# Performance work log

Measured on AMD Instinct MI355X. Metric: run time of the kernel, lower is better.

The kernel has to match this reference:

```python
import jax, jax.numpy as jnp
import numpy as np

HEADS = 8
DIM_HEAD = 64
GAMMA = 0.01
LAMBDA_REG = 0.001
EPS = 1e-6


def layer_norm(x, g, b, eps=1e-5):
    mu = x.mean(-1, keepdims=True)
    var = jnp.var(x, axis=-1, keepdims=True)
    return (x - mu) * jax.lax.rsqrt(var + eps) * g + b


def setup_inputs() -> dict:
    key = jax.random.key(0)
    ks = jax.random.split(key, 20)
    B, N, DIM = 8, 1024, 512
    d = DIM_HEAD
    inner = HEADS * d
    inp = {}
    inp["q"] = jax.random.normal(ks[0], (B, N, DIM), jnp.float32)
    inp["k"] = jax.random.normal(ks[1], (B, N, DIM), jnp.float32)
    inp["v"] = jax.random.normal(ks[2], (B, N, DIM), jnp.float32)
    # input_linear: LayerNorm(dim) + Linear(dim -> inner, no bias)
    inp["ln_g"] = jnp.ones((DIM,), jnp.float32)
    inp["ln_b"] = jnp.zeros((DIM,), jnp.float32)
    inp["W_in"] = jax.random.normal(ks[3], (DIM, inner), jnp.float32) * 0.02
    # weight_predictor: Linear(2d->d), LN(d), ReLU, Linear(d->d//2), ReLU, Linear(d//2->3), Softmax
    inp["wp_W1"] = jax.random.normal(ks[4], (2 * d, d), jnp.float32) * 0.05
    inp["wp_b1"] = jnp.zeros((d,), jnp.float32)
    inp["wp_ln_g"] = jnp.ones((d,), jnp.float32)
    inp["wp_ln_b"] = jnp.zeros((d,), jnp.float32)
    inp["wp_W2"] = jax.random.normal(ks[5], (d, d // 2), jnp.float32) * 0.05
    inp["wp_b2"] = jnp.zeros((d // 2,), jnp.float32)
    inp["wp_W3"] = jax.random.normal(ks[6], (d // 2, 3), jnp.float32) * 0.05
    inp["wp_b3"] = jnp.zeros((3,), jnp.float32)
    inp["weight_temp"] = jnp.ones((1,), jnp.float32) * 2.0
    # output_linear: Linear(inner -> dim) with bias
    inp["W_out"] = jax.random.normal(ks[7], (inner, DIM), jnp.float32) * 0.02
    inp["b_out"] = jnp.zeros((DIM,), jnp.float32)
    return inp


def reference(q, k, v, ln_g, ln_b, W_in, wp_W1, wp_b1, wp_ln_g, wp_ln_b,
              wp_W2, wp_b2, wp_W3, wp_b3, weight_temp, W_out, b_out):
    H, d = HEADS, DIM_HEAD
    B, N, _ = q.shape

    def proj(t):
        x = layer_norm(t, ln_g, ln_b) @ W_in          # [B, N, H*d]
        return x.reshape(B, N, H, d).transpose(2, 0, 1, 3)  # h q n d

    f_q, f_k, f_v = proj(q), proj(k), proj(v)
    m = f_k.shape[2]

    # --- cosine component (cosine_distance with clamp to [-0.95, 0.95]) ---
    dots_raw = jnp.einsum('hbnd,hbmd->hbnm', f_q, f_k)
    n1 = jnp.linalg.norm(f_q, axis=-1, keepdims=True) + EPS      # h b n 1
    n2 = jnp.linalg.norm(f_k, axis=-1) + EPS                      # h b m
    cosine_sim = jnp.clip(dots_raw / (n1 * n2[:, :, None, :]), -0.95, 0.95)

    # --- regularized covariance component ---
    f_k_c = f_k - f_k.mean(axis=2, keepdims=True)
    f_q_c = f_q - f_q.mean(axis=-1, keepdims=True)
    cov = jnp.einsum('hbnd,hbmd->hbnm', f_q_c, f_k_c) / (d ** 0.5 + 1e-6)
    cov = jnp.clip((LAMBDA_REG / max(m, 1)) * cov, -20.0, 20.0)

    # --- margin-based variance component (eval: adaptive_gamma == gamma) ---
    fqn = f_q / jnp.maximum(jnp.linalg.norm(f_q, axis=-1, keepdims=True), EPS)
    fkn = f_k / jnp.maximum(jnp.linalg.norm(f_k, axis=-1, keepdims=True), EPS)
    cs = jnp.clip(jnp.einsum('hbnd,hbmd->hbnm', fqn, fkn), -0.95, 0.95)
    margin = jnp.clip(GAMMA - cs, 0.0, 5.0)
    var_full = jnp.broadcast_to(margin.mean(axis=-1, keepdims=True), cs.shape)

    # --- dynamic weight mixing ---
    q_g = f_q.mean(axis=(1, 2))   # [h, d]
    k_g = f_k.mean(axis=(1, 2))
    z = jnp.concatenate([q_g, k_g], axis=-1) @ wp_W1 + wp_b1
    z = jax.nn.relu(layer_norm(z, wp_ln_g, wp_ln_b))
    z = jax.nn.relu(z @ wp_W2 + wp_b2)
    p = jax.nn.softmax(z @ wp_W3 + wp_b3, axis=-1)   # predictor ends with Softmax
    wt = jnp.clip(weight_temp, 0.1, 10.0)
    w = jax.nn.softmax(p / wt, axis=-1)               # second softmax, as in torch
    w = w * (1.0 - 3 * 0.1) + 0.1                     # [h, 3]
    cw = w[:, 0][:, None, None, None]
    covw = w[:, 1][:, None, None, None]
    vw = w[:, 2][:, None, None, None]

    sg = jax.lax.stop_gradient
    std1 = lambda x: jnp.std(x, ddof=1)               # torch.std is unbiased
    cos_n = sg(std1(cosine_sim)) + EPS
    cov_n = sg(std1(cov)) + EPS
    var_n = sg(std1(var_full)) + EPS

    dots = cw * (cosine_sim / cos_n) + covw * (cov / cov_n * 0.3) + vw * (var_full / var_n * 0.3)
    temp = jnp.clip(0.5 + sg(std1(dots)), 0.3, 3.0)
    dots = dots / temp

    out = jnp.einsum('hbnm,hbmd->hbnd', jax.nn.softmax(dots, axis=-1), f_v)
    out = out.transpose(1, 2, 0, 3).reshape(B, N, H * d)
    return out @ W_out + b_out
```

## Files before the change

### kernel.cpp

```cpp
#include <hip/hip_runtime.h>
#include <math.h>

#define H_ 8
#define B_ 8
#define N_ 1024
#define D_ 64
#define DIMM 512
#define NROWS 8192

typedef __attribute__((ext_vector_type(8))) short s8v;
typedef __attribute__((ext_vector_type(4))) float f4v;
typedef __attribute__((ext_vector_type(2))) unsigned int u2v;
union fragu { s8v v; unsigned int w[4]; uint4 q; };

#define BMFMA(a, b, c) __builtin_amdgcn_mfma_f32_16x16x32_bf16(a, b, c, 0, 0, 0)
#define FMED3(x, lo, hi) __builtin_amdgcn_fmed3f((x), (lo), (hi))

__device__ __forceinline__ float wred_sum(float v) {
#pragma unroll
    for (int m = 32; m >= 1; m >>= 1) v += __shfl_xor(v, m, 64);
    return v;
}
__device__ __forceinline__ double wred_sum_d(double v) {
#pragma unroll
    for (int m = 32; m >= 1; m >>= 1) v += __shfl_xor(v, m, 64);
    return v;
}
__device__ __forceinline__ float b2f(unsigned short h) {
    return __uint_as_float(((unsigned)h) << 16);
}
__device__ __forceinline__ unsigned cvtpk(float a, float b) {
    unsigned r;
    asm("v_cvt_pk_bf16_f32 %0, %1, %2" : "=v"(r) : "v"(a), "v"(b));
    return r;
}
__device__ __forceinline__ void bsplit(float a, unsigned short& hi, unsigned short& lo) {
    unsigned h = cvtpk(a, 0.f);
    hi = (unsigned short)h;
    float r = a - __uint_as_float(h << 16);
    lo = (unsigned short)cvtpk(r, 0.f);
}
__device__ __forceinline__ void split8(const float* a, unsigned* hw, unsigned* lw) {
#pragma unroll
    for (int i = 0; i < 4; ++i) {
        unsigned h = cvtpk(a[2 * i], a[2 * i + 1]);
        hw[i] = h;
        float l0 = a[2 * i]     - __uint_as_float(h << 16);
        float l1 = a[2 * i + 1] - __uint_as_float(h & 0xFFFF0000u);
        lw[i] = cvtpk(l0, l1);
    }
}

__device__ __forceinline__ float fexp2(float x) {
#if __has_builtin(__builtin_amdgcn_exp2f)
    return __builtin_amdgcn_exp2f(x);
#else
    return exp2f(x);
#endif
}

#if __has_builtin(__builtin_amdgcn_permlane16_swap) && __has_builtin(__builtin_amdgcn_permlane32_swap)
#define HAVE_PLSWAP 1
#endif

__device__ __forceinline__ float kbmax4(float x) {
#ifdef HAVE_PLSWAP
    u2v a = __builtin_amdgcn_permlane16_swap(__float_as_uint(x), __float_as_uint(x), false, false);
    float m = fmaxf(__uint_as_float(a[0]), __uint_as_float(a[1]));
    u2v c = __builtin_amdgcn_permlane32_swap(__float_as_uint(m), __float_as_uint(m), false, false);
    return fmaxf(__uint_as_float(c[0]), __uint_as_float(c[1]));
#else
    x = fmaxf(x, __shfl_xor(x, 16, 64));
    return fmaxf(x, __shfl_xor(x, 32, 64));
#endif
}
__device__ __forceinline__ float kbsum4(float x) {
#ifdef HAVE_PLSWAP
    u2v a = __builtin_amdgcn_permlane16_swap(__float_as_uint(x), __float_as_uint(x), false, false);
    float m = __uint_as_float(a[0]) + __uint_as_float(a[1]);
    u2v c = __builtin_amdgcn_permlane32_swap(__float_as_uint(m), __float_as_uint(m), false, false);
    return __uint_as_float(c[0]) + __uint_as_float(c[1]);
#else
    x += __shfl_xor(x, 16, 64);
    x += __shfl_xor(x, 32, 64);
    return x;
#endif
}

__global__ __launch_bounds__(256) void k_lnstats(
    const float* __restrict__ q, const float* __restrict__ k, const float* __restrict__ v,
    float* __restrict__ muv, float* __restrict__ rsd)
{
    int t = threadIdx.x;
    int w = t >> 6, lane = t & 63;
    int row = blockIdx.x * 4 + w;
    int tens = row >> 13;
    int lrow = row & 8191;
    const float* src = (tens == 0) ? q : (tens == 1 ? k : v);
    const float* p = src + (long long)lrow * DIMM + lane * 8;
    float4 a = *(const float4*)p;
    float4 b = *(const float4*)(p + 4);
    float s  = a.x + a.y + a.z + a.w + b.x + b.y + b.z + b.w;
    float sq = a.x*a.x + a.y*a.y + a.z*a.z + a.w*a.w + b.x*b.x + b.y*b.y + b.z*b.z + b.w*b.w;
    s = wred_sum(s); sq = wred_sum(sq);
    if (lane == 0) {
        float m = s * (1.f / 512.f);
        float var = sq * (1.f / 512.f) - m * m;
        muv[row] = m;
        rsd[row] = rsqrtf(var + 1e-5f);
    }
}

__global__ __launch_bounds__(256) void k_splitW(
    const float* __restrict__ Win, const float* __restrict__ Wout,
    unsigned short* __restrict__ Wthi, unsigned short* __restrict__ Wtlo,
    unsigned short* __restrict__ Wothi, unsigned short* __restrict__ Wotlo)
{
    const float* Wsrc = blockIdx.z ? Wout : Win;
    unsigned short* Dhi = blockIdx.z ? Wothi : Wthi;
    unsigned short* Dlo = blockIdx.z ? Wotlo : Wtlo;
    int k0 = blockIdx.x * 64, j0 = blockIdx.y * 64;
    __shared__ float S[64][65];
    int t = threadIdx.x, rr = t >> 2, seg = t & 3;
    const float* p = Wsrc + (long long)(k0 + rr) * DIMM + j0 + seg * 16;
    float4 a0 = *(const float4*)p, a1 = *(const float4*)(p + 4),
           a2 = *(const float4*)(p + 8), a3 = *(const float4*)(p + 12);
    S[rr][seg*16+ 0]=a0.x; S[rr][seg*16+ 1]=a0.y; S[rr][seg*16+ 2]=a0.z; S[rr][seg*16+ 3]=a0.w;
    S[rr][seg*16+ 4]=a1.x; S[rr][seg*16+ 5]=a1.y; S[rr][seg*16+ 6]=a1.z; S[rr][seg*16+ 7]=a1.w;
    S[rr][seg*16+ 8]=a2.x; S[rr][seg*16+ 9]=a2.y; S[rr][seg*16+10]=a2.z; S[rr][seg*16+11]=a2.w;
    S[rr][seg*16+12]=a3.x; S[rr][seg*16+13]=a3.y; S[rr][seg*16+14]=a3.z; S[rr][seg*16+15]=a3.w;
    __syncthreads();
    float f[16];
#pragma unroll
    for (int i = 0; i < 16; ++i) f[i] = S[seg * 16 + i][rr];
    unsigned hw[8], lw[8];
    split8(f, hw, lw);
    split8(f + 8, hw + 4, lw + 4);
    long long ob = (long long)(j0 + rr) * DIMM + k0 + seg * 16;
    *(uint4*)&Dhi[ob]     = make_uint4(hw[0], hw[1], hw[2], hw[3]);
    *(uint4*)&Dhi[ob + 8] = make_uint4(hw[4], hw[5], hw[6], hw[7]);
    *(uint4*)&Dlo[ob]     = make_uint4(lw[0], lw[1], lw[2], lw[3]);
    *(uint4*)&Dlo[ob + 8] = make_uint4(lw[4], lw[5], lw[6], lw[7]);
}

__global__ __launch_bounds__(256) void k_gemm_in(
    const float* __restrict__ qx, const float* __restrict__ kx, const float* __restrict__ vx,
    const float* __restrict__ muv, const float* __restrict__ rsd,
    const float* __restrict__ lng, const float* __restrict__ lnb,
    const unsigned short* __restrict__ Wthi, const unsigned short* __restrict__ Wtlo,
    unsigned short* __restrict__ Fqhi, unsigned short* __restrict__ Fqlo,
    unsigned short* __restrict__ Fkhi, unsigned short* __restrict__ Fklo,
    unsigned short* __restrict__ Fvthi, unsigned short* __restrict__ Fvtlo,
    float* __restrict__ qinv, float* __restrict__ mq,
    float* __restrict__ kinv, float* __restrict__ ks,
    float* __restrict__ csq, float* __restrict__ csk)
{
    int tens = blockIdx.z;
    const float* X = (tens == 0) ? qx : (tens == 1 ? kx : vx);
    int row0 = blockIdx.x * 128, hq = blockIdx.y;
    const float* muT = muv + tens * NROWS;
    const float* rsT = rsd + tens * NROWS;
    __shared__ unsigned short Ah[128][32], Al[128][32];
    __shared__ unsigned short Bh[128][32], Bl[128][32];
    int t = threadIdx.x;
    int w = t >> 6, lane = t & 63, l15 = lane & 15, kb = lane >> 4;
    int srow = t >> 1, sseg = t & 1;
    int sw = (srow >> 1) & 3;
    int c0 = ((2 * sseg + 0) ^ sw) * 8;
    int c1 = ((2 * sseg + 1) ^ sw) * 8;
    int rs = (l15 >> 1) & 3;
    int rb = (kb ^ rs) * 8;
    float amu = muT[row0 + srow], ars = rsT[row0 + srow];
    f4v acc[2][8];
#pragma unroll
    for (int rt = 0; rt < 2; ++rt)
#pragma unroll
        for (int dt = 0; dt < 8; ++dt) acc[rt][dt] = (f4v){0.f, 0.f, 0.f, 0.f};

    float4 x0, x1, x2, x3, g0, g1, g2, g3, cc0, cc1, cc2, cc3;
    uint4 wh0, wh1, wl0, wl1;
#define GIN_LOAD(KC) { \
    int kO = (KC) * 32 + sseg * 16; \
    const float* xp = X + (long long)(row0 + srow) * DIMM + kO; \
    x0 = *(const float4*)xp;       x1 = *(const float4*)(xp + 4); \
    x2 = *(const float4*)(xp + 8); x3 = *(const float4*)(xp + 12); \
    g0 = *(const float4*)(lng + kO);     g1 = *(const float4*)(lng + kO + 4); \
    g2 = *(const float4*)(lng + kO + 8); g3 = *(const float4*)(lng + kO + 12); \
    cc0 = *(const float4*)(lnb + kO);     cc1 = *(const float4*)(lnb + kO + 4); \
    cc2 = *(const float4*)(lnb + kO + 8); cc3 = *(const float4*)(lnb + kO + 12); \
    const unsigned short* wph = Wthi + (long long)(hq * 128 + srow) * DIMM + kO; \
    const unsigned short* wpl = Wtlo + (long long)(hq * 128 + srow) * DIMM + kO; \
    wh0 = *(const uint4*)wph; wh1 = *(const uint4*)(wph + 8); \
    wl0 = *(const uint4*)wpl; wl1 = *(const uint4*)(wpl + 8); }

    GIN_LOAD(0)
    for (int kc = 0; kc < 16; ++kc) {
        float av[16];
        av[ 0]=fmaf((x0.x-amu)*ars,g0.x,cc0.x); av[ 1]=fmaf((x0.y-amu)*ars,g0.y,cc0.y);
        av[ 2]=fmaf((x0.z-amu)*ars,g0.z,cc0.z); av[ 3]=fmaf((x0.w-amu)*ars,g0.w,cc0.w);
        av[ 4]=fmaf((x1.x-amu)*ars,g1.x,cc1.x); av[ 5]=fmaf((x1.y-amu)*ars,g1.y,cc1.y);
        av[ 6]=fmaf((x1.z-amu)*ars,g1.z,cc1.z); av[ 7]=fmaf((x1.w-amu)*ars,g1.w,cc1.w);
        av[ 8]=fmaf((x2.x-amu)*ars,g2.x,cc2.x); av[ 9]=fmaf((x2.y-amu)*ars,g2.y,cc2.y);
        av[10]=fmaf((x2.z-amu)*ars,g2.z,cc2.z); av[11]=fmaf((x2.w-amu)*ars,g2.w,cc2.w);
        av[12]=fmaf((x3.x-amu)*ars,g3.x,cc3.x); av[13]=fmaf((x3.y-amu)*ars,g3.y,cc3.y);
        av[14]=fmaf((x3.z-amu)*ars,g3.z,cc3.z); av[15]=fmaf((x3.w-amu)*ars,g3.w,cc3.w);
        unsigned hw[8], lw[8];
        split8(av, hw, lw);
        split8(av + 8, hw + 4, lw + 4);
        *(uint4*)&Ah[srow][c0] = make_uint4(hw[0], hw[1], hw[2], hw[3]);
        *(uint4*)&Ah[srow][c1] = make_uint4(hw[4], hw[5], hw[6], hw[7]);
        *(uint4*)&Al[srow][c0] = make_uint4(lw[0], lw[1], lw[2], lw[3]);
        *(uint4*)&Al[srow][c1] = make_uint4(lw[4], lw[5], lw[6], lw[7]);
        *(uint4*)&Bh[srow][c0] = wh0;
        *(uint4*)&Bh[srow][c1] = wh1;
        *(uint4*)&Bl[srow][c0] = wl0;
        *(uint4*)&Bl[srow][c1] = wl1;
        __syncthreads();
        if (kc < 15) { GIN_LOAD(kc + 1) }
        fragu ah[2], al2[2];
#pragma unroll
        for (int rt = 0; rt < 2; ++rt) {
            ah[rt].v  = *(const s8v*)&Ah[w * 32 + rt * 16 + l15][rb];
            al2[rt].v = *(const s8v*)&Al[w * 32 + rt * 16 + l15][rb];
        }
#pragma unroll
        for (int dt = 0; dt < 8; ++dt) {
            s8v bh = *(const s8v*)&Bh[dt * 16 + l15][rb];
            s8v bl = *(const s8v*)&Bl[dt * 16 + l15][rb];
#pragma unroll
            for (int rt = 0; rt < 2; ++rt) {
                acc[rt][dt] = BMFMA(ah[rt].v, bh, acc[rt][dt]);
                acc[rt][dt] = BMFMA(ah[rt].v, bl, acc[rt][dt]);
                acc[rt][dt] = BMFMA(al2[rt].v, bh, acc[rt][dt]);
            }
        }
        __syncthreads();
    }
#undef GIN_LOAD
    int b = row0 >> 10;
    if (tens < 2) {
        unsigned short* Dh = tens ? Fkhi : Fqhi;
        unsigned short* Dl = tens ? Fklo : Fqlo;
#pragma unroll
        for (int rt = 0; rt < 2; ++rt) {
            int nloc = (row0 & 1023) + w * 32 + rt * 16 + kb * 4;
#pragma unroll
            for (int dt = 0; dt < 8; ++dt) {
                int hb = (hq * 2 + (dt >> 2)) * 8 + b;
#pragma unroll
                for (int r = 0; r < 4; ++r) {
                    unsigned short hi, lo;
                    bsplit(acc[rt][dt][r], hi, lo);
                    long long idx = ((long long)hb * N_ + nloc + r) * D_ + (dt & 3) * 16 + l15;
                    Dh[idx] = hi;
                    Dl[idx] = lo;
                }
            }
#pragma unroll
            for (int hh = 0; hh < 2; ++hh) {
                int hb2 = (hq * 2 + hh) * 8 + b;
#pragma unroll
                for (int r = 0; r < 4; ++r) {
                    float a0 = acc[rt][hh*4+0][r], a1 = acc[rt][hh*4+1][r],
                          a2 = acc[rt][hh*4+2][r], a3 = acc[rt][hh*4+3][r];
                    float s  = a0 + a1 + a2 + a3;
                    float sq = a0*a0 + a1*a1 + a2*a2 + a3*a3;
#pragma unroll
                    for (int msk = 8; msk >= 1; msk >>= 1) {
                        s  += __shfl_xor(s, msk, 64);
                        sq += __shfl_xor(sq, msk, 64);
                    }
                    if (l15 == 0) {
                        int rowg = hb2 * N_ + nloc + r;
                        float inv = 1.f / (sqrtf(sq) + 1e-6f);
                        if (tens) { kinv[rowg] = inv; ks[rowg] = s; }
                        else      { qinv[rowg] = inv; mq[rowg] = s * (1.f / 64.f); }
// ... 179 lines not shown
        long long qbase = ((long long)hb * N_ + n0 + w * 16 + l15) * D_;
#pragma unroll
        for (int k2 = 0; k2 < 2; ++k2)
            qh[k2].q = *(const uint4*)(Fqhi + qbase + k2 * 32 + kb * 8);
    }
    float qi1_r[4], qm_r[4], qgs_r[4];
#pragma unroll
    for (int r = 0; r < 4; ++r) {
        int rowg = hb * N_ + n0 + w * 16 + kb * 4 + r;
        qi1_r[r] = qinvA[rowg];
        qm_r[r]  = mqA[rowg];
        qgs_r[r] = gA[rowg] * SC;
    }
    float sacc[5][4] = {};

    for (int mt = mtc * 4; mt < mtc * 4 + 4; ++mt) {
        {
            long long kro = ((long long)hb * N_ + mt * 64 + srow) * D_ + seg * 16;
            uint4 h0 = *(const uint4*)(Fkhi + kro), h1 = *(const uint4*)(Fkhi + kro + 8);
            *(uint4*)&Khi[srow][seg * 16]     = h0;
            *(uint4*)&Khi[srow][seg * 16 + 8] = h1;
            if (t < 64) {
                ki1s[t] = kinvA[hb * N_ + mt * 64 + t];
                ksls[t] = ksA[hb * N_ + mt * 64 + t];
            }
        }
        __syncthreads();
#pragma unroll
        for (int nt = 0; nt < 4; ++nt) {
            f4v acc = {0.f, 0.f, 0.f, 0.f};
            s8v kh0 = *(const s8v*)&Khi[nt * 16 + l15][kb * 8];
            s8v kh1 = *(const s8v*)&Khi[nt * 16 + l15][32 + kb * 8];
            acc = BMFMA(qh[0].v, kh0, acc);
            acc = BMFMA(qh[1].v, kh1, acc);
            int key = nt * 16 + l15;
            float k1 = ki1s[key];
            float ksvSC = ksls[key] * SC;
            float e_r[4];
#pragma unroll
            for (int r = 0; r < 4; ++r) e_r[r] = fmaf(qm_r[r], ksvSC, qgs_r[r]);
#pragma unroll
            for (int r = 0; r < 4; ++r) {
                float dv = acc[r];
                float A  = FMED3(dv * qi1_r[r] * k1, -0.95f, 0.95f);
                float Bv = fmaf(dv, SC, -e_r[r]);
                sacc[0][r] += A;
                sacc[1][r] = fmaf(A, A, sacc[1][r]);
                sacc[2][r] = fmaf(Bv, Bv, sacc[2][r]);
                sacc[3][r] = fmaf(A, Bv, sacc[3][r]);
                sacc[4][r] += fminf(A, 0.01f);
            }
        }
        __syncthreads();
    }
    {
        const int map[4] = {0, 3, 4, 6};
#pragma unroll
        for (int qq = 0; qq < 4; ++qq) {
            float s = sacc[qq][0] + sacc[qq][1] + sacc[qq][2] + sacc[qq][3];
            double d = wred_sum_d((double)s);
            if (lane == 0) wsum[qq][w] = d;
        }
        __syncthreads();
        if (t < 4) {
            double tot = wsum[t][0] + wsum[t][1] + wsum[t][2] + wsum[t][3];
            atomicAdd(&accum[h * 9 + map[t]], tot);
        }
    }
    float vA[4], vM[4];
#pragma unroll
    for (int r = 0; r < 4; ++r) {
        float a = sacc[0][r], m = sacc[4][r];
#pragma unroll
        for (int msk = 8; msk >= 1; msk >>= 1) {
            a += __shfl_xor(a, msk, 64);
            m += __shfl_xor(m, msk, 64);
        }
        vA[r] = a; vM[r] = m;
    }
    if (l15 == 0) {
#pragma unroll
        for (int r = 0; r < 4; ++r) {
            int rowg = hb * N_ + n0 + w * 16 + kb * 4 + r;
            atomicAdd(&rowA[rowg], vA[r]);
            atomicAdd(&rowM[rowg], 2.56f - vM[r]);
        }
    }
}

__global__ __launch_bounds__(256) void k_rowfin(
    const float* __restrict__ rowA, const float* __restrict__ rowB,
    const float* __restrict__ rowM, float* __restrict__ varC,
    double* __restrict__ accum)
{
    (void)rowB;
    int hb = blockIdx.x;
    int h = hb >> 3;
    int t = threadIdx.x;
    int w = t >> 6, lane = t & 63;
    __shared__ double wsum[3][4];
    double c2 = 0, c5 = 0, c7 = 0;
    for (int i = t; i < N_; i += 256) {
        int idx = hb * N_ + i;
        float rm = rowM[idx];
        float C = rm * (1.f / 1024.f);
        varC[idx] = C;
        c2 += (double)rm;
        c5 += (double)rm * (double)C;
        c7 += (double)C * (double)rowA[idx];
    }
    c2 = wred_sum_d(c2); c5 = wred_sum_d(c5); c7 = wred_sum_d(c7);
    if (lane == 0) { wsum[0][w] = c2; wsum[1][w] = c5; wsum[2][w] = c7; }
    __syncthreads();
    if (t < 3) {
        const int map[3] = {2, 5, 7};
        double tot = wsum[t][0] + wsum[t][1] + wsum[t][2] + wsum[t][3];
        atomicAdd(&accum[h * 9 + map[t]], tot);
    }
}

__global__ void k_fin(const double* __restrict__ accum, const float* __restrict__ wbuf,
                      float* __restrict__ scl)
{
    if (threadIdx.x != 0) return;
    const double T = 67108864.0;
    double GA=0, GB=0, GC=0, GAA=0, GBB=0, GCC=0;
    for (int h = 0; h < 8; ++h) {
        GA  += accum[h*9+0]; GB  += accum[h*9+1]; GC  += accum[h*9+2];
        GAA += accum[h*9+3]; GBB += accum[h*9+4]; GCC += accum[h*9+5];
    }
    double cos_n = sqrt(fmax((GAA - GA*GA/T) / (T - 1.0), 0.0)) + 1e-6;
    double cov_n = sqrt(fmax((GBB - GB*GB/T) / (T - 1.0), 0.0)) + 1e-6;
    double var_n = sqrt(fmax((GCC - GC*GC/T) / (T - 1.0), 0.0)) + 1e-6;
    double sd = 0, sd2 = 0;
    double al[8], be[8], ga[8];
    for (int h = 0; h < 8; ++h) {
        al[h] = (double)wbuf[h*3+0] / cos_n;
        be[h] = (double)wbuf[h*3+1] * 0.3 / cov_n;
        ga[h] = (double)wbuf[h*3+2] * 0.3 / var_n;
        sd  += al[h]*accum[h*9+0] + be[h]*accum[h*9+1] + ga[h]*accum[h*9+2];
        sd2 += al[h]*al[h]*accum[h*9+3] + be[h]*be[h]*accum[h*9+4] + ga[h]*ga[h]*accum[h*9+5]
             + 2.0*al[h]*be[h]*accum[h*9+6] + 2.0*al[h]*ga[h]*accum[h*9+7] + 2.0*be[h]*ga[h]*accum[h*9+8];
    }
    double vard = fmax((sd2 - sd*sd/T) / (T - 1.0), 0.0);
    double temp = 0.5 + sqrt(vard);
    temp = fmin(fmax(temp, 0.3), 3.0);
    for (int h = 0; h < 8; ++h) {
        scl[h*3+0] = (float)(al[h] / temp);
        scl[h*3+1] = (float)(be[h] / temp);
        scl[h*3+2] = (float)(ga[h] / temp);
    }
}

__global__ __launch_bounds__(512) void k_pass2(
    const unsigned short* __restrict__ Fqhi, const unsigned short* __restrict__ Fqlo,
    const unsigned short* __restrict__ Fkhi, const unsigned short* __restrict__ Fklo,
    const unsigned short* __restrict__ Fvthi, const unsigned short* __restrict__ Fvtlo,
    const float* __restrict__ qinvA, const float* __restrict__ mqA, const float* __restrict__ gA,
    const float* __restrict__ kinvA, const float* __restrict__ ksA,
    const float* __restrict__ varC, const float* __restrict__ scl,
    unsigned short* __restrict__ attn_hi, unsigned short* __restrict__ attn_lo)
{
    int bx = blockIdx.x;
    int g = bx >> 3;
    int hb = (bx & 7) * 8 + (g >> 3);
    int n0 = (g & 7) * 128;
    int h = hb >> 3, b = hb & 7;
    __shared__ unsigned short Khi[2][64][72];
    __shared__ unsigned short Klo[2][64][72];
    __shared__ unsigned short Vh[2][64][72];
    __shared__ unsigned short Vl[2][64][72];
    __shared__ float ki1s[2][64], ksls[2][64];
    int t = threadIdx.x;
    int w = t >> 6, lane = t & 63, l15 = lane & 15, kb = lane >> 4;
    int srow = t >> 3, sc = (t & 7) * 8;
    const float SC = (float)((0.001 / 1024.0) / (8.0 + 1e-6));
    const float L2E = 1.44269504f;
    float sAh = scl[h*3+0] * L2E, sBh = scl[h*3+1] * L2E, sCh = scl[h*3+2] * L2E;

    fragu qh[2], ql[2];
    {
        long long qbase = ((long long)hb * N_ + n0 + w * 16 + l15) * D_;
#pragma unroll
        for (int k2 = 0; k2 < 2; ++k2) {
            qh[k2].q = *(const uint4*)(Fqhi + qbase + k2 * 32 + kb * 8);
            ql[k2].q = *(const uint4*)(Fqlo + qbase + k2 * 32 + kb * 8);
        }
    }
    int rowq = hb * N_ + n0 + w * 16 + l15;
    float qiA = qinvA[rowq] * sAh;
    float qm  = mqA[rowq];
    float c95 = 0.95f * sAh;
    float SCb = SC * sBh;
    float cb  = fmaf(sCh, varC[rowq], -(gA[rowq] * SC) * sBh);

    float Mr = -1e30f, Lr = 0.f;
    f4v oacc[4];
#pragma unroll
    for (int dt = 0; dt < 4; ++dt) oacc[dt] = (f4v){0.f, 0.f, 0.f, 0.f};
    int idxr[4];
#pragma unroll
    for (int r = 0; r < 4; ++r) idxr[r] = (kb * 20 + r) * 4;

    uint4 rkh, rkl, rvh, rvl;
    float rki, rks;
#define P2_LOAD(MT) { \
    long long kro = ((long long)hb * N_ + (MT) * 64 + srow) * D_ + sc; \
    rkh = *(const uint4*)(Fkhi + kro); rkl = *(const uint4*)(Fklo + kro); \
    long long vro = ((long long)hb * D_ + srow) * N_ + (MT) * 64 + sc; \
    rvh = *(const uint4*)(Fvthi + vro); rvl = *(const uint4*)(Fvtlo + vro); \
    if (t < 64) { rki = kinvA[hb * N_ + (MT) * 64 + t]; rks = ksA[hb * N_ + (MT) * 64 + t]; } }

    P2_LOAD(0)
    for (int mt = 0; mt < 16; ++mt) {
        int buf = mt & 1;
        *(uint4*)&Khi[buf][srow][sc] = rkh;
        *(uint4*)&Klo[buf][srow][sc] = rkl;
        *(uint4*)&Vh[buf][srow][sc]  = rvh;
        *(uint4*)&Vl[buf][srow][sc]  = rvl;
        if (t < 64) { ki1s[buf][t] = rki; ksls[buf][t] = rks; }
        __syncthreads();
        if (mt < 15) { P2_LOAD(mt + 1) }
        float p[4][4];
#pragma unroll
        for (int nt = 0; nt < 4; ++nt) {
            f4v acc = {0.f, 0.f, 0.f, 0.f};
            __builtin_amdgcn_s_setprio(1);
#pragma unroll
            for (int k2 = 0; k2 < 2; ++k2) {
                s8v kh = *(const s8v*)&Khi[buf][nt * 16 + l15][k2 * 32 + kb * 8];
                s8v kl = *(const s8v*)&Klo[buf][nt * 16 + l15][k2 * 32 + kb * 8];
                acc = BMFMA(kh, qh[k2].v, acc);
                acc = BMFMA(kh, ql[k2].v, acc);
                acc = BMFMA(kl, qh[k2].v, acc);
            }
            __builtin_amdgcn_s_setprio(0);
            float4 k1v = *(const float4*)&ki1s[buf][nt * 16 + kb * 4];
            float4 ksv = *(const float4*)&ksls[buf][nt * 16 + kb * 4];
            float qk[4]  = {qiA * k1v.x, qiA * k1v.y, qiA * k1v.z, qiA * k1v.w};
            float ksa[4] = {ksv.x, ksv.y, ksv.z, ksv.w};
#pragma unroll
            for (int r = 0; r < 4; ++r) {
                float dv = acc[r];
                float A  = FMED3(dv * qk[r], -c95, c95);
                float u  = fmaf(-qm, ksa[r], dv);
                p[nt][r] = fmaf(u, SCb, A + cb);
            }
        }
        float tmax = fmaxf(fmaxf(fmaxf(p[0][0], p[0][1]), fmaxf(p[0][2], p[0][3])),
                           fmaxf(fmaxf(p[1][0], p[1][1]), fmaxf(p[1][2], p[1][3])));
        tmax = fmaxf(tmax, fmaxf(fmaxf(fmaxf(p[2][0], p[2][1]), fmaxf(p[2][2], p[2][3])),
                                 fmaxf(fmaxf(p[3][0], p[3][1]), fmaxf(p[3][2], p[3][3]))));
        tmax = kbmax4(tmax);
        if (__any(tmax - Mr > 11.5415605f)) {
            float nM = fmaxf(Mr, tmax);
            float scf = fexp2(Mr - nM);
            Mr = nM;
            Lr *= scf;
            float scr[4];
#pragma unroll
            for (int r = 0; r < 4; ++r)
                scr[r] = __int_as_float(__builtin_amdgcn_ds_bpermute(idxr[r], __float_as_int(scf)));
#pragma unroll
            for (int dt = 0; dt < 4; ++dt)
#pragma unroll
                for (int r = 0; r < 4; ++r) oacc[dt][r] *= scr[r];
        }
        float ps = 0.f;
#pragma unroll
        for (int nt = 0; nt < 4; ++nt)
#pragma unroll
            for (int r = 0; r < 4; ++r) {
                float e = fexp2(p[nt][r] - Mr);
                p[nt][r] = e;
                ps += e;
            }
        ps = kbsum4(ps);
        Lr += ps;
        fragu pah[2], pal[2];
#pragma unroll
        for (int k2 = 0; k2 < 2; ++k2) {
#pragma unroll
            for (int j = 0; j < 4; ++j) {
                float x = p[2 * k2 + (j >> 1)][(j & 1) * 2];
                float y = p[2 * k2 + (j >> 1)][(j & 1) * 2 + 1];
                unsigned hw2 = cvtpk(x, y);
                pah[k2].w[j] = hw2;
                float lx = x - __uint_as_float(hw2 << 16);
                float ly = y - __uint_as_float(hw2 & 0xFFFF0000u);
                pal[k2].w[j] = cvtpk(lx, ly);
            }
        }
        __builtin_amdgcn_s_setprio(1);
#pragma unroll
        for (int dt = 0; dt < 4; ++dt) {
#pragma unroll
            for (int k2 = 0; k2 < 2; ++k2) {
                s8v vh2 = *(const s8v*)&Vh[buf][dt * 16 + l15][k2 * 32 + kb * 8];
                s8v vl2 = *(const s8v*)&Vl[buf][dt * 16 + l15][k2 * 32 + kb * 8];
                oacc[dt] = BMFMA(pah[k2].v, vh2, oacc[dt]);
                oacc[dt] = BMFMA(pah[k2].v, vl2, oacc[dt]);
                oacc[dt] = BMFMA(pal[k2].v, vh2, oacc[dt]);
            }
        }
        __builtin_amdgcn_s_setprio(0);
    }
#undef P2_LOAD
    float inv_r[4];
#pragma unroll
    for (int r = 0; r < 4; ++r) {
        float Lq = __int_as_float(__builtin_amdgcn_ds_bpermute(idxr[r], __float_as_int(Lr)));
        inv_r[r] = 1.f / Lq;
    }
#pragma unroll
    for (int dt = 0; dt < 4; ++dt)
#pragma unroll
        for (int r = 0; r < 4; ++r) {
            float o = oacc[dt][r] * inv_r[r];
            unsigned short hi, lo;
            bsplit(o, hi, lo);
            long long idx = ((long long)(b * N_ + n0 + w * 16 + kb * 4 + r)) * DIMM + h * 64 + dt * 16 + l15;
            attn_hi[idx] = hi;
            attn_lo[idx] = lo;
        }
}

__global__ __launch_bounds__(256) void k_gemm_out(
    const unsigned short* __restrict__ Ahi, const unsigned short* __restrict__ Alo,
    const unsigned short* __restrict__ Wothi, const unsigned short* __restrict__ Wotlo,
    const float* __restrict__ bias, float* __restrict__ out)
{
    int row0 = blockIdx.x * 128, j0 = blockIdx.y * 128;
    __shared__ unsigned short Ah[128][32], Al[128][32];
    __shared__ unsigned short Bh[128][32], Bl[128][32];
    int t = threadIdx.x;
    int w = t >> 6, lane = t & 63, l15 = lane & 15, kb = lane >> 4;
    int srow = t >> 1, sseg = t & 1;
    int sw = (srow >> 1) & 3;
    int c0 = ((2 * sseg + 0) ^ sw) * 8;
    int c1 = ((2 * sseg + 1) ^ sw) * 8;
    int rs = (l15 >> 1) & 3;
    int rb = (kb ^ rs) * 8;
    f4v acc[2][8];
#pragma unroll
    for (int rt = 0; rt < 2; ++rt)
#pragma unroll
        for (int dt = 0; dt < 8; ++dt) acc[rt][dt] = (f4v){0.f, 0.f, 0.f, 0.f};
    uint4 a0, a1, al0, al1, b0, b1, bl0, bl1;
#define GOUT_LOAD(KC) { \
    int kO = (KC) * 32 + sseg * 16; \
    const unsigned short* ap  = Ahi + (long long)(row0 + srow) * DIMM + kO; \
    const unsigned short* alp = Alo + (long long)(row0 + srow) * DIMM + kO; \
    a0 = *(const uint4*)ap;  a1 = *(const uint4*)(ap + 8); \
    al0 = *(const uint4*)alp; al1 = *(const uint4*)(alp + 8); \
    const unsigned short* bp  = Wothi + (long long)(j0 + srow) * DIMM + kO; \
    const unsigned short* blp = Wotlo + (long long)(j0 + srow) * DIMM + kO; \
    b0 = *(const uint4*)bp;  b1 = *(const uint4*)(bp + 8); \
    bl0 = *(const uint4*)blp; bl1 = *(const uint4*)(blp + 8); }

    GOUT_LOAD(0)
    for (int kc = 0; kc < 16; ++kc) {
        *(uint4*)&Ah[srow][c0] = a0;
        *(uint4*)&Ah[srow][c1] = a1;
        *(uint4*)&Al[srow][c0] = al0;
        *(uint4*)&Al[srow][c1] = al1;
        *(uint4*)&Bh[srow][c0] = b0;
        *(uint4*)&Bh[srow][c1] = b1;
        *(uint4*)&Bl[srow][c0] = bl0;
        *(uint4*)&Bl[srow][c1] = bl1;
        __syncthreads();
        if (kc < 15) { GOUT_LOAD(kc + 1) }
        fragu ah[2], al2[2];
#pragma unroll
        for (int rt = 0; rt < 2; ++rt) {
            ah[rt].v  = *(const s8v*)&Ah[w * 32 + rt * 16 + l15][rb];
            al2[rt].v = *(const s8v*)&Al[w * 32 + rt * 16 + l15][rb];
        }
#pragma unroll
        for (int dt = 0; dt < 8; ++dt) {
            s8v bh = *(const s8v*)&Bh[dt * 16 + l15][rb];
            s8v bl = *(const s8v*)&Bl[dt * 16 + l15][rb];
#pragma unroll
            for (int rt = 0; rt < 2; ++rt) {
                acc[rt][dt] = BMFMA(ah[rt].v, bh, acc[rt][dt]);
                acc[rt][dt] = BMFMA(ah[rt].v, bl, acc[rt][dt]);
                acc[rt][dt] = BMFMA(al2[rt].v, bh, acc[rt][dt]);
            }
        }
        __syncthreads();
    }
#undef GOUT_LOAD
#pragma unroll
    for (int dt = 0; dt < 8; ++dt) {
        float bv = bias[j0 + dt * 16 + l15];
#pragma unroll
        for (int rt = 0; rt < 2; ++rt)
#pragma unroll
            for (int r = 0; r < 4; ++r)
                out[(long long)(row0 + w * 32 + rt * 16 + kb * 4 + r) * DIMM + j0 + dt * 16 + l15]
                    = acc[rt][dt][r] + bv;
    }
}

extern "C" void kernel_launch(void* const* d_in, const int* in_sizes, int n_in,
                              void* d_out, int out_size, void* d_ws, size_t ws_size,
                              hipStream_t stream) {
    (void)in_sizes; (void)n_in; (void)out_size; (void)ws_size;
    const float* q      = (const float*)d_in[0];
    const float* k      = (const float*)d_in[1];
    const float* v      = (const float*)d_in[2];
    const float* ln_g   = (const float*)d_in[3];
    const float* ln_b   = (const float*)d_in[4];
    const float* W_in   = (const float*)d_in[5];
    const float* wp_W1  = (const float*)d_in[6];
    const float* wp_b1  = (const float*)d_in[7];
    const float* wp_lng = (const float*)d_in[8];
    const float* wp_lnb = (const float*)d_in[9];
    const float* wp_W2  = (const float*)d_in[10];
    const float* wp_b2  = (const float*)d_in[11];
    const float* wp_W3  = (const float*)d_in[12];
    const float* wp_b3  = (const float*)d_in[13];
    const float* wtemp  = (const float*)d_in[14];
    const float* W_out  = (const float*)d_in[15];
    const float* b_out  = (const float*)d_in[16];
    float* out = (float*)d_out;

    char* w = (char*)d_ws;
    unsigned short* attn_hi = (unsigned short*)(w + 0);
    unsigned short* attn_lo = (unsigned short*)(w + 8388608);
    unsigned short* Fqhi  = (unsigned short*)(w + 16777216);
    unsigned short* Fqlo  = (unsigned short*)(w + 25165824);
    unsigned short* Fkhi  = (unsigned short*)(w + 33554432);
    unsigned short* Fklo  = (unsigned short*)(w + 41943040);
    unsigned short* Fvthi = (unsigned short*)(w + 50331648);
    unsigned short* Fvtlo = (unsigned short*)(w + 58720256);
    unsigned short* Wthi  = (unsigned short*)(w + 67108864);
    unsigned short* Wtlo  = (unsigned short*)(w + 67633152);
    unsigned short* Wothi = (unsigned short*)(w + 68157440);
    unsigned short* Wotlo = (unsigned short*)(w + 68681728);
    float* muv  = (float*)(w + 69206016);
    float* rsd  = (float*)(w + 69304320);
    float* qinv = (float*)(w + 69402624);
    float* mq   = (float*)(w + 69664768);
    float* gv   = (float*)(w + 69926912);
    float* kinv = (float*)(w + 70189056);
    float* ks   = (float*)(w + 70451200);
    float* vc   = (float*)(w + 70713344);
    float* rowA = (float*)(w + 70975488);
    float* rowB = (float*)(w + 71237632);
    float* rowM = (float*)(w + 71499776);
    float* csq  = (float*)(w + 71761920);
    float* csk  = (float*)(w + 71778304);
    double* acc = (double*)(w + 71794688);
    float* wb   = (float*)(w + 71796736);
    float* scl  = (float*)(w + 71796864);

    hipMemsetAsync(rowA, 0, 3 * 262144 + 2 * 16384 + 2048, stream);

    k_lnstats<<<6144, 256, 0, stream>>>(q, k, v, muv, rsd);
    k_splitW<<<dim3(8, 8, 2), 256, 0, stream>>>(W_in, W_out, Wthi, Wtlo, Wothi, Wotlo);
    k_gemm_in<<<dim3(64, 4, 3), 256, 0, stream>>>(q, k, v, muv, rsd, ln_g, ln_b,
                                                  Wthi, Wtlo, Fqhi, Fqlo, Fkhi, Fklo, Fvthi, Fvtlo,
                                                  qinv, mq, kinv, ks, csq, csk);
    k_gvec<<<256, 256, 0, stream>>>(Fqhi, Fqlo, csk, mq, gv);
    k_mlp<<<1, 512, 0, stream>>>(csq, csk, wp_W1, wp_b1, wp_lng, wp_lnb, wp_W2, wp_b2, wp_W3, wp_b3, wtemp, wb);
    k_pass1<<<4096, 256, 0, stream>>>(Fqhi, Fkhi, qinv, mq, gv, kinv, ks, rowA, rowB, rowM, acc);
    k_rowfin<<<64, 256, 0, stream>>>(rowA, rowB, rowM, vc, acc);
    k_fin<<<1, 64, 0, stream>>>(acc, wb, scl);
    k_pass2<<<512, 512, 0, stream>>>(Fqhi, Fqlo, Fkhi, Fklo, Fvthi, Fvtlo,
                                     qinv, mq, gv, kinv, ks, vc, scl, attn_hi, attn_lo);
    k_gemm_out<<<dim3(64, 4), 256, 0, stream>>>(attn_hi, attn_lo, Wothi, Wotlo, b_out, out);
}
```

Baseline: 225.9 us.

## Process two query row-groups per wave in pass2 and merge prep kernels

The flash-style pass2 kernel now runs 4 waves of 256 threads instead of 8 waves, with each wave handling two 16-row query groups. Every K/V fragment read from shared memory is therefore reused across twice as many MFMAs, and each thread stages two rows of K/V per tile. Separately, the layernorm-stats and weight-split kernels are merged into one launch to save a kernel launch. The trade-off is more registers per thread (doubled accumulators and Q fragments) and fewer waves per block to hide latency.

```diff
diff --git a/kernel.cpp b/kernel.cpp
--- a/kernel.cpp
+++ b/kernel.cpp
@@ -87,41 +87,45 @@
 #endif
 }
 
-__global__ __launch_bounds__(256) void k_lnstats(
+__global__ __launch_bounds__(256) void k_prep(
     const float* __restrict__ q, const float* __restrict__ k, const float* __restrict__ v,
-    float* __restrict__ muv, float* __restrict__ rsd)
-{
-    int t = threadIdx.x;
-    int w = t >> 6, lane = t & 63;
-    int row = blockIdx.x * 4 + w;
-    int tens = row >> 13;
-    int lrow = row & 8191;
-    const float* src = (tens == 0) ? q : (tens == 1 ? k : v);
-    const float* p = src + (long long)lrow * DIMM + lane * 8;
-    float4 a = *(const float4*)p;
-    float4 b = *(const float4*)(p + 4);
-    float s  = a.x + a.y + a.z + a.w + b.x + b.y + b.z + b.w;
-    float sq = a.x*a.x + a.y*a.y + a.z*a.z + a.w*a.w + b.x*b.x + b.y*b.y + b.z*b.z + b.w*b.w;
-    s = wred_sum(s); sq = wred_sum(sq);
-    if (lane == 0) {
-        float m = s * (1.f / 512.f);
-        float var = sq * (1.f / 512.f) - m * m;
-        muv[row] = m;
-        rsd[row] = rsqrtf(var + 1e-5f);
-    }
-}
-
-__global__ __launch_bounds__(256) void k_splitW(
+    float* __restrict__ muv, float* __restrict__ rsd,
     const float* __restrict__ Win, const float* __restrict__ Wout,
     unsigned short* __restrict__ Wthi, unsigned short* __restrict__ Wtlo,
     unsigned short* __restrict__ Wothi, unsigned short* __restrict__ Wotlo)
 {
-    const float* Wsrc = blockIdx.z ? Wout : Win;
-    unsigned short* Dhi = blockIdx.z ? Wothi : Wthi;
-    unsigned short* Dlo = blockIdx.z ? Wotlo : Wtlo;
-    int k0 = blockIdx.x * 64, j0 = blockIdx.y * 64;
+    int bx = blockIdx.x;
     __shared__ float S[64][65];
-    int t = threadIdx.x, rr = t >> 2, seg = t & 3;
+    int t = threadIdx.x;
+    if (bx < 6144) {
+        int w = t >> 6, lane = t & 63;
+        int row = bx * 4 + w;
+        int tens = row >> 13;
+        int lrow = row & 8191;
+        const float* src = (tens == 0) ? q : (tens == 1 ? k : v);
+        const float* p = src + (long long)lrow * DIMM + lane * 8;
+        float4 a = *(const float4*)p;
+        float4 b = *(const float4*)(p + 4);
+        float s  = a.x + a.y + a.z + a.w + b.x + b.y + b.z + b.w;
+        float sq = a.x*a.x + a.y*a.y + a.z*a.z + a.w*a.w + b.x*b.x + b.y*b.y + b.z*b.z + b.w*b.w;
+        s = wred_sum(s); sq = wred_sum(sq);
+        if (lane == 0) {
+            float m = s * (1.f / 512.f);
+            float var = sq * (1.f / 512.f) - m * m;
+            muv[row] = m;
+            rsd[row] = rsqrtf(var + 1e-5f);
+        }
+        return;
+    }
+    int sb = bx - 6144;
+    int z = sb >> 6;
+    int rem = sb & 63;
+    int kxi = rem & 7, jxi = rem >> 3;
+    const float* Wsrc = z ? Wout : Win;
+    unsigned short* Dhi = z ? Wothi : Wthi;
+    unsigned short* Dlo = z ? Wotlo : Wtlo;
+    int k0 = kxi * 64, j0 = jxi * 64;
+    int rr = t >> 2, seg = t & 3;
     const float* p = Wsrc + (long long)(k0 + rr) * DIMM + j0 + seg * 16;
     float4 a0 = *(const float4*)p, a1 = *(const float4*)(p + 4),
            a2 = *(const float4*)(p + 8), a3 = *(const float4*)(p + 12);
@@ -607,7 +611,7 @@
     }
 }
 
-__global__ __launch_bounds__(512) void k_pass2(
+__global__ __launch_bounds__(256, 2) void k_pass2(
     const unsigned short* __restrict__ Fqhi, const unsigned short* __restrict__ Fqlo,
     const unsigned short* __restrict__ Fkhi, const unsigned short* __restrict__ Fklo,
     const unsigned short* __restrict__ Fvthi, const unsigned short* __restrict__ Fvtlo,
@@ -632,118 +636,139 @@
     const float SC = (float)((0.001 / 1024.0) / (8.0 + 1e-6));
     const float L2E = 1.44269504f;
     float sAh = scl[h*3+0] * L2E, sBh = scl[h*3+1] * L2E, sCh = scl[h*3+2] * L2E;
-
-    fragu qh[2], ql[2];
-    {
-        long long qbase = ((long long)hb * N_ + n0 + w * 16 + l15) * D_;
-#pragma unroll
-        for (int k2 = 0; k2 < 2; ++k2) {
-            qh[k2].q = *(const uint4*)(Fqhi + qbase + k2 * 32 + kb * 8);
-            ql[k2].q = *(const uint4*)(Fqlo + qbase + k2 * 32 + kb * 8);
-        }
-    }
-    int rowq = hb * N_ + n0 + w * 16 + l15;
-    float qiA = qinvA[rowq] * sAh;
-    float qm  = mqA[rowq];
     float c95 = 0.95f * sAh;
     float SCb = SC * sBh;
-    float cb  = fmaf(sCh, varC[rowq], -(gA[rowq] * SC) * sBh);
-
-    float Mr = -1e30f, Lr = 0.f;
-    f4v oacc[4];
-#pragma unroll
-    for (int dt = 0; dt < 4; ++dt) oacc[dt] = (f4v){0.f, 0.f, 0.f, 0.f};
+
+    fragu qh[2][2], ql[2][2];
+    float qiA[2], qm[2], cb[2];
+#pragma unroll
+    for (int rg = 0; rg < 2; ++rg) {
+        int rowq = hb * N_ + n0 + w * 32 + rg * 16 + l15;
+        long long qbase = (long long)rowq * D_;
+#pragma unroll
+        for (int k2 = 0; k2 < 2; ++k2) {
+            qh[rg][k2].q = *(const uint4*)(Fqhi + qbase + k2 * 32 + kb * 8);
+            ql[rg][k2].q = *(const uint4*)(Fqlo + qbase + k2 * 32 + kb * 8);
+        }
+        qiA[rg] = qinvA[rowq] * sAh;
+        qm[rg]  = mqA[rowq];
+        cb[rg]  = fmaf(sCh, varC[rowq], -(gA[rowq] * SC) * sBh);
+    }
+
+    float Mr[2] = {-1e30f, -1e30f}, Lr[2] = {0.f, 0.f};
+    f4v oacc[2][4];
+#pragma unroll
+    for (int rg = 0; rg < 2; ++rg)
+#pragma unroll
+        for (int dt = 0; dt < 4; ++dt) oacc[rg][dt] = (f4v){0.f, 0.f, 0.f, 0.f};
     int idxr[4];
 #pragma unroll
     for (int r = 0; r < 4; ++r) idxr[r] = (kb * 20 + r) * 4;
 
-    uint4 rkh, rkl, rvh, rvl;
+    uint4 rkh[2], rkl[2], rvh[2], rvl[2];
     float rki, rks;
 #define P2_LOAD(MT) { \
-    long long kro = ((long long)hb * N_ + (MT) * 64 + srow) * D_ + sc; \
-    rkh = *(const uint4*)(Fkhi + kro); rkl = *(const uint4*)(Fklo + kro); \
-    long long vro = ((long long)hb * D_ + srow) * N_ + (MT) * 64 + sc; \
-    rvh = *(const uint4*)(Fvthi + vro); rvl = *(const uint4*)(Fvtlo + vro); \
+    _Pragma("unroll") \
+    for (int j = 0; j < 2; ++j) { \
+        long long kro = ((long long)hb * N_ + (MT) * 64 + srow + j * 32) * D_ + sc; \
+        rkh[j] = *(const uint4*)(Fkhi + kro); rkl[j] = *(const uint4*)(Fklo + kro); \
+        long long vro = ((long long)hb * D_ + srow + j * 32) * N_ + (MT) * 64 + sc; \
+        rvh[j] = *(const uint4*)(Fvthi + vro); rvl[j] = *(const uint4*)(Fvtlo + vro); \
+    } \
     if (t < 64) { rki = kinvA[hb * N_ + (MT) * 64 + t]; rks = ksA[hb * N_ + (MT) * 64 + t]; } }
 
     P2_LOAD(0)
     for (int mt = 0; mt < 16; ++mt) {
         int buf = mt & 1;
-        *(uint4*)&Khi[buf][srow][sc] = rkh;
-        *(uint4*)&Klo[buf][srow][sc] = rkl;
-        *(uint4*)&Vh[buf][srow][sc]  = rvh;
-        *(uint4*)&Vl[buf][srow][sc]  = rvl;
+#pragma unroll
+        for (int j = 0; j < 2; ++j) {
+            *(uint4*)&Khi[buf][srow + j * 32][sc] = rkh[j];
+            *(uint4*)&Klo[buf][srow + j * 32][sc] = rkl[j];
+            *(uint4*)&Vh[buf][srow + j * 32][sc]  = rvh[j];
+            *(uint4*)&Vl[buf][srow + j * 32][sc]  = rvl[j];
+        }
         if (t < 64) { ki1s[buf][t] = rki; ksls[buf][t] = rks; }
         __syncthreads();
         if (mt < 15) { P2_LOAD(mt + 1) }
-        float p[4][4];
+        float p[2][4][4];
 #pragma unroll
         for (int nt = 0; nt < 4; ++nt) {
-            f4v acc = {0.f, 0.f, 0.f, 0.f};
+            f4v a0 = {0.f, 0.f, 0.f, 0.f};
+            f4v a1 = {0.f, 0.f, 0.f, 0.f};
             __builtin_amdgcn_s_setprio(1);
 #pragma unroll
             for (int k2 = 0; k2 < 2; ++k2) {
                 s8v kh = *(const s8v*)&Khi[buf][nt * 16 + l15][k2 * 32 + kb * 8];
                 s8v kl = *(const s8v*)&Klo[buf][nt * 16 + l15][k2 * 32 + kb * 8];
-                acc = BMFMA(kh, qh[k2].v, acc);
-                acc = BMFMA(kh, ql[k2].v, acc);
-                acc = BMFMA(kl, qh[k2].v, acc);
+                a0 = BMFMA(kh, qh[0][k2].v, a0);
+                a0 = BMFMA(kh, ql[0][k2].v, a0);
+                a0 = BMFMA(kl, qh[0][k2].v, a0);
+                a1 = BMFMA(kh, qh[1][k2].v, a1);
+                a1 = BMFMA(kh, ql[1][k2].v, a1);
+                a1 = BMFMA(kl, qh[1][k2].v, a1);
             }
             __builtin_amdgcn_s_setprio(0);
             float4 k1v = *(const float4*)&ki1s[buf][nt * 16 + kb * 4];
             float4 ksv = *(const float4*)&ksls[buf][nt * 16 + kb * 4];
-            float qk[4]  = {qiA * k1v.x, qiA * k1v.y, qiA * k1v.z, qiA * k1v.w};
+            float k1a[4] = {k1v.x, k1v.y, k1v.z, k1v.w};
             float ksa[4] = {ksv.x, ksv.y, ksv.z, ksv.w};
 #pragma unroll
             for (int r = 0; r < 4; ++r) {
-                float dv = acc[r];
-                float A  = FMED3(dv * qk[r], -c95, c95);
-                float u  = fmaf(-qm, ksa[r], dv);
-                p[nt][r] = fmaf(u, SCb, A + cb);
-            }
-        }
-        float tmax = fmaxf(fmaxf(fmaxf(p[0][0], p[0][1]), fmaxf(p[0][2], p[0][3])),
-                           fmaxf(fmaxf(p[1][0], p[1][1]), fmaxf(p[1][2], p[1][3])));
-        tmax = fmaxf(tmax, fmaxf(fmaxf(fmaxf(p[2][0], p[2][1]), fmaxf(p[2][2], p[2][3])),
-                                 fmaxf(fmaxf(p[3][0], p[3][1]), fmaxf(p[3][2], p[3][3]))));
-        tmax = kbmax4(tmax);
-        if (__any(tmax - Mr > 11.5415605f)) {
-            float nM = fmaxf(Mr, tmax);
-            float scf = fexp2(Mr - nM);
-            Mr = nM;
-            Lr *= scf;
-            float scr[4];
-#pragma unroll
-            for (int r = 0; r < 4; ++r)
-                scr[r] = __int_as_float(__builtin_amdgcn_ds_bpermute(idxr[r], __float_as_int(scf)));
-#pragma unroll
-            for (int dt = 0; dt < 4; ++dt)
-#pragma unroll
-                for (int r = 0; r < 4; ++r) oacc[dt][r] *= scr[r];
-        }
-        float ps = 0.f;
-#pragma unroll
-        for (int nt = 0; nt < 4; ++nt)
-#pragma unroll
-            for (int r = 0; r < 4; ++r) {
-                float e = fexp2(p[nt][r] - Mr);
-                p[nt][r] = e;
-                ps += e;
-            }
-        ps = kbsum4(ps);
-        Lr += ps;
-        fragu pah[2], pal[2];
-#pragma unroll
-        for (int k2 = 0; k2 < 2; ++k2) {
-#pragma unroll
-            for (int j = 0; j < 4; ++j) {
-                float x = p[2 * k2 + (j >> 1)][(j & 1) * 2];
-                float y = p[2 * k2 + (j >> 1)][(j & 1) * 2 + 1];
-                unsigned hw2 = cvtpk(x, y);
-                pah[k2].w[j] = hw2;
-                float lx = x - __uint_as_float(hw2 << 16);
-                float ly = y - __uint_as_float(hw2 & 0xFFFF0000u);
-                pal[k2].w[j] = cvtpk(lx, ly);
+                float dv0 = a0[r];
+                float A0  = FMED3(dv0 * (qiA[0] * k1a[r]), -c95, c95);
+                float u0  = fmaf(-qm[0], ksa[r], dv0);
+                p[0][nt][r] = fmaf(u0, SCb, A0 + cb[0]);
+                float dv1 = a1[r];
+                float A1  = FMED3(dv1 * (qiA[1] * k1a[r]), -c95, c95);
+                float u1  = fmaf(-qm[1], ksa[r], dv1);
+                p[1][nt][r] = fmaf(u1, SCb, A1 + cb[1]);
+            }
+        }
+        fragu pah[2][2], pal[2][2];
+#pragma unroll
+        for (int rg = 0; rg < 2; ++rg) {
+            float tmax = fmaxf(fmaxf(fmaxf(p[rg][0][0], p[rg][0][1]), fmaxf(p[rg][0][2], p[rg][0][3])),
+                               fmaxf(fmaxf(p[rg][1][0], p[rg][1][1]), fmaxf(p[rg][1][2], p[rg][1][3])));
+            tmax = fmaxf(tmax, fmaxf(fmaxf(fmaxf(p[rg][2][0], p[rg][2][1]), fmaxf(p[rg][2][2], p[rg][2][3])),
+                                     fmaxf(fmaxf(p[rg][3][0], p[rg][3][1]), fmaxf(p[rg][3][2], p[rg][3][3]))));
+            tmax = kbmax4(tmax);
+            if (__any(tmax - Mr[rg] > 11.5415605f)) {
+                float nM = fmaxf(Mr[rg], tmax);
+                float scf = fexp2(Mr[rg] - nM);
+                Mr[rg] = nM;
+                Lr[rg] *= scf;
+                float scr[4];
+#pragma unroll
+                for (int r = 0; r < 4; ++r)
+                    scr[r] = __int_as_float(__builtin_amdgcn_ds_bpermute(idxr[r], __float_as_int(scf)));
+#pragma unroll
+                for (int dt = 0; dt < 4; ++dt)
+#pragma unroll
+                    for (int r = 0; r < 4; ++r) oacc[rg][dt][r] *= scr[r];
+            }
+            float ps = 0.f;
+#pragma unroll
+            for (int nt = 0; nt < 4; ++nt)
+#pragma unroll
+                for (int r = 0; r < 4; ++r) {
+                    float e = fexp2(p[rg][nt][r] - Mr[rg]);
+                    p[rg][nt][r] = e;
+                    ps += e;
+                }
+            ps = kbsum4(ps);
+            Lr[rg] += ps;
+#pragma unroll
+            for (int k2 = 0; k2 < 2; ++k2) {
+#pragma unroll
+                for (int j = 0; j < 4; ++j) {
+                    float x = p[rg][2 * k2 + (j >> 1)][(j & 1) * 2];
+                    float y = p[rg][2 * k2 + (j >> 1)][(j & 1) * 2 + 1];
+                    unsigned hw2 = cvtpk(x, y);
+                    pah[rg][k2].w[j] = hw2;
+                    float lx = x - __uint_as_float(hw2 << 16);
+                    float ly = y - __uint_as_float(hw2 & 0xFFFF0000u);
+                    pal[rg][k2].w[j] = cvtpk(lx, ly);
+                }
             }
         }
         __builtin_amdgcn_s_setprio(1);
@@ -753,31 +778,38 @@
             for (int k2 = 0; k2 < 2; ++k2) {
                 s8v vh2 = *(const s8v*)&Vh[buf][dt * 16 + l15][k2 * 32 + kb * 8];
                 s8v vl2 = *(const s8v*)&Vl[buf][dt * 16 + l15][k2 * 32 + kb * 8];
-                oacc[dt] = BMFMA(pah[k2].v, vh2, oacc[dt]);
-                oacc[dt] = BMFMA(pah[k2].v, vl2, oacc[dt]);
-                oacc[dt] = BMFMA(pal[k2].v, vh2, oacc[dt]);
+                oacc[0][dt] = BMFMA(pah[0][k2].v, vh2, oacc[0][dt]);
+                oacc[0][dt] = BMFMA(pah[0][k2].v, vl2, oacc[0][dt]);
+                oacc[0][dt] = BMFMA(pal[0][k2].v, vh2, oacc[0][dt]);
+                oacc[1][dt] = BMFMA(pah[1][k2].v, vh2, oacc[1][dt]);
+                oacc[1][dt] = BMFMA(pah[1][k2].v, vl2, oacc[1][dt]);
+                oacc[1][dt] = BMFMA(pal[1][k2].v, vh2, oacc[1][dt]);
             }
         }
         __builtin_amdgcn_s_setprio(0);
     }
 #undef P2_LOAD
-    float inv_r[4];
-#pragma unroll
-    for (int r = 0; r < 4; ++r) {
-        float Lq = __int_as_float(__builtin_amdgcn_ds_bpermute(idxr[r], __float_as_int(Lr)));
-        inv_r[r] = 1.f / Lq;
-    }
-#pragma unroll
-    for (int dt = 0; dt < 4; ++dt)
+#pragma unroll
+    for (int rg = 0; rg < 2; ++rg) {
+        float inv_r[4];
 #pragma unroll
         for (int r = 0; r < 4; ++r) {
-            float o = oacc[dt][r] * inv_r[r];
-            unsigned short hi, lo;
-            bsplit(o, hi, lo);
-            long long idx = ((long long)(b * N_ + n0 + w * 16 + kb * 4 + r)) * DIMM + h * 64 + dt * 16 + l15;
-            attn_hi[idx] = hi;
-            attn_lo[idx] = lo;
-        }
+            float Lq = __int_as_float(__builtin_amdgcn_ds_bpermute(idxr[r], __float_as_int(Lr[rg])));
+            inv_r[r] = 1.f / Lq;
+        }
+#pragma unroll
+        for (int dt = 0; dt < 4; ++dt)
+#pragma unroll
+            for (int r = 0; r < 4; ++r) {
+                float o = oacc[rg][dt][r] * inv_r[r];
+                unsigned short hi, lo;
+                bsplit(o, hi, lo);
+                long long idx = ((long long)(b * N_ + n0 + w * 32 + rg * 16 + kb * 4 + r)) * DIMM
+                              + h * 64 + dt * 16 + l15;
+                attn_hi[idx] = hi;
+                attn_lo[idx] = lo;
+            }
+    }
 }
 
 __global__ __launch_bounds__(256) void k_gemm_out(
@@ -912,8 +944,7 @@
 
     hipMemsetAsync(rowA, 0, 3 * 262144 + 2 * 16384 + 2048, stream);
 
-    k_lnstats<<<6144, 256, 0, stream>>>(q, k, v, muv, rsd);
-    k_splitW<<<dim3(8, 8, 2), 256, 0, stream>>>(W_in, W_out, Wthi, Wtlo, Wothi, Wotlo);
+    k_prep<<<6272, 256, 0, stream>>>(q, k, v, muv, rsd, W_in, W_out, Wthi, Wtlo, Wothi, Wotlo);
     k_gemm_in<<<dim3(64, 4, 3), 256, 0, stream>>>(q, k, v, muv, rsd, ln_g, ln_b,
                                                   Wthi, Wtlo, Fqhi, Fqlo, Fkhi, Fklo, Fvthi, Fvtlo,
                                                   qinv, mq, kinv, ks, csq, csk);
@@ -922,7 +953,7 @@
     k_pass1<<<4096, 256, 0, stream>>>(Fqhi, Fkhi, qinv, mq, gv, kinv, ks, rowA, rowB, rowM, acc);
     k_rowfin<<<64, 256, 0, stream>>>(rowA, rowB, rowM, vc, acc);
     k_fin<<<1, 64, 0, stream>>>(acc, wb, scl);
-    k_pass2<<<512, 512, 0, stream>>>(Fqhi, Fqlo, Fkhi, Fklo, Fvthi, Fvtlo,
+    k_pass2<<<512, 256, 0, stream>>>(Fqhi, Fqlo, Fkhi, Fklo, Fvthi, Fvtlo,
                                      qinv, mq, gv, kinv, ks, vc, scl, attn_hi, attn_lo);
     k_gemm_out<<<dim3(64, 4), 256, 0, stream>>>(attn_hi, attn_lo, Wothi, Wotlo, b_out, out);
 }
```

Result: slower. 260.4 us (+15.2%).
